# Optimization experiments

Hardware: AMD Instinct MI355X
Metric: run time of the kernel (lower is better)

## Reference

```python
import jax, jax.numpy as jnp
import numpy as np

SEQ_LEN = 8192
HEAD_DIM = 128


def setup_inputs() -> dict:
    key = jax.random.key(0)
    kq, kk, kv = jax.random.split(key, 3)
    q = jax.random.normal(kq, (SEQ_LEN, HEAD_DIM), dtype=jnp.float32)
    k = jax.random.normal(kk, (SEQ_LEN, HEAD_DIM), dtype=jnp.float32)
    v = jax.random.normal(kv, (SEQ_LEN, HEAD_DIM), dtype=jnp.float32)
    return {"q": q, "k": k, "v": v}


def reference(q, k, v):
    # FlashAttention computes exact softmax attention; the blocked loops with
    # online max/sum rescaling in the source are an exact reformulation of:
    #   O = softmax(Q K^T) V
    # NOTE: the original module applies no 1/sqrt(d) scaling, so neither do we.
    s = jnp.einsum('nd,md->nm', q, k)          # [N, N] scores
    p = jax.nn.softmax(s, axis=-1)             # stable softmax (online in src)
    return jnp.einsum('nm,md->nd', p, v)       # [N, d]
```

## Files before the change

### kernel.cpp

```cpp
#include <hip/hip_runtime.h>

#define N_SEQ 8192
#define HDIM  128

typedef _Float16 half8v  __attribute__((ext_vector_type(8)));
typedef float    floatx16 __attribute__((ext_vector_type(16)));
typedef unsigned int uint32;

__global__ void prep_kv(const float* __restrict__ K, const float* __restrict__ V,
                        _Float16* __restrict__ K16s, _Float16* __restrict__ Vs) {
    __shared__ float Kl[32 * 132];
    __shared__ float Vl[32 * 132];
    const int t  = threadIdx.x;
    const int nt = blockIdx.x;
    const int n0 = nt * 32;
    #pragma unroll
    for (int kk = 0; kk < 4; kk++) {
        int idx = t + 256 * kk;
        int nl = idx >> 5, c4 = idx & 31;
        float4 f = *(((const float4*)(K + (size_t)(n0 + nl) * HDIM)) + c4);
        float* dk = &Kl[nl * 132 + c4 * 4];
        dk[0] = f.x; dk[1] = f.y; dk[2] = f.z; dk[3] = f.w;
        float4 g = *(((const float4*)(V + (size_t)(n0 + nl) * HDIM)) + c4);
        float* dv = &Vl[nl * 132 + c4 * 4];
        dv[0] = g.x; dv[1] = g.y; dv[2] = g.z; dv[3] = g.w;
    }
    __syncthreads();
    #pragma unroll
    for (int rep = 0; rep < 2; rep++) {
        int ch = t + rep * 256;
        int kc = ch >> 6, lane = ch & 63, l31 = lane & 31, q5 = (lane >> 5) & 1;
        half8v h;
        #pragma unroll
        for (int j = 0; j < 8; j++) h[j] = (_Float16)Kl[l31 * 132 + kc * 16 + q5 * 8 + j];
        *(half8v*)(K16s + (((size_t)nt * 8 + kc) * 64 + lane) * 8) = h;
    }
    #pragma unroll
    for (int rep = 0; rep < 2; rep++) {
        int ch = t + rep * 256;
        int dt = ch >> 7, kc2 = (ch >> 6) & 1, lane = ch & 63, l31 = lane & 31, q5 = (lane >> 5) & 1;
        half8v h;
        #pragma unroll
        for (int j = 0; j < 8; j++) h[j] = (_Float16)Vl[(kc2 * 16 + q5 * 8 + j) * 132 + dt * 32 + l31];
        *(half8v*)(Vs + ((((size_t)nt * 4 + dt) * 2 + kc2) * 64 + lane) * 8) = h;
    }
}

__launch_bounds__(256, 2)
__global__ void fa_main(const float* __restrict__ Qp, const _Float16* __restrict__ K16s,
                        const _Float16* __restrict__ Vs, float* __restrict__ Opart,
                        float* __restrict__ lpart, float* __restrict__ mpart, int tiles) {
    const int tid  = threadIdx.x;
    const int lane = tid & 63;
    const int wv   = tid >> 6;
    const int l31  = lane & 31;
    const int q5   = lane >> 5;
    const int m0   = blockIdx.x * 128 + wv * 32;
    const int sp   = blockIdx.y;
    const float LOG2E = 1.44269504088896f;

    half8v qf[8];
    {
        const float* qrow = Qp + (size_t)(m0 + l31) * HDIM;
        #pragma unroll
        for (int kc = 0; kc < 8; kc++) {
            const float4 a = *(const float4*)(qrow + kc * 16 + q5 * 8);
            const float4 b = *(const float4*)(qrow + kc * 16 + q5 * 8 + 4);
            half8v h;
            h[0] = (_Float16)(a.x * LOG2E); h[1] = (_Float16)(a.y * LOG2E);
            h[2] = (_Float16)(a.z * LOG2E); h[3] = (_Float16)(a.w * LOG2E);
            h[4] = (_Float16)(b.x * LOG2E); h[5] = (_Float16)(b.y * LOG2E);
            h[6] = (_Float16)(b.z * LOG2E); h[7] = (_Float16)(b.w * LOG2E);
            qf[kc] = h;
        }
    }

    floatx16 oacc[4];
    #pragma unroll
    for (int dt = 0; dt < 4; dt++)
        #pragma unroll
        for (int r = 0; r < 16; r++) oacc[dt][r] = 0.0f;

    float runm = -3.0e38f;
    float lsum = 0.0f;

    const int nt0 = sp * tiles;
    for (int it = 0; it < tiles; ++it) {
        const size_t nt = nt0 + it;
        half8v vf[8];
        #pragma unroll
        for (int dt = 0; dt < 4; dt++)
            #pragma unroll
            for (int kc2 = 0; kc2 < 2; kc2++)
                vf[dt * 2 + kc2] = *(const half8v*)(Vs + (((nt * 4 + dt) * 2 + kc2) * 64 + lane) * 8);
        half8v kf[8];
        #pragma unroll
        for (int kc = 0; kc < 8; kc++)
            kf[kc] = *(const half8v*)(K16s + ((nt * 8 + kc) * 64 + lane) * 8);
        floatx16 s0, s1;
        #pragma unroll
        for (int r = 0; r < 16; r++) { s0[r] = 0.0f; s1[r] = 0.0f; }
        #pragma unroll
        for (int kc = 0; kc < 4; kc++)
            s0 = __builtin_amdgcn_mfma_f32_32x32x16_f16(kf[kc], qf[kc], s0, 0, 0, 0);
        #pragma unroll
        for (int kc = 4; kc < 8; kc++)
            s1 = __builtin_amdgcn_mfma_f32_32x32x16_f16(kf[kc], qf[kc], s1, 0, 0, 0);
        float sc[16];
        #pragma unroll
        for (int r = 0; r < 16; r++) sc[r] = s0[r] + s1[r];
        float tm[8];
        #pragma unroll
        for (int r = 0; r < 8; r++) tm[r] = fmaxf(sc[r], sc[r + 8]);
        #pragma unroll
        for (int w = 4; w; w >>= 1)
            #pragma unroll
            for (int r = 0; r < w; r++) tm[r] = fmaxf(tm[r], tm[r + w]);
        float cmax = fmaxf(tm[0], __shfl_xor(tm[0], 32, 64));
        if (__any(cmax > runm + 12.0f)) {
            const float mnew  = fmaxf(runm, cmax);
            const float alpha = __builtin_amdgcn_exp2f(runm - mnew);
            runm = mnew;
            lsum *= alpha;
            #pragma unroll
            for (int dt = 0; dt < 4; dt++)
                #pragma unroll
                for (int r = 0; r < 16; r++) oacc[dt][r] *= alpha;
        }
        float p[16];
        #pragma unroll
        for (int r = 0; r < 16; r++) p[r] = __builtin_amdgcn_exp2f(sc[r] - runm);
        float ts[8];
        #pragma unroll
        for (int r = 0; r < 8; r++) ts[r] = p[r] + p[r + 8];
        #pragma unroll
        for (int w = 4; w; w >>= 1)
            #pragma unroll
            for (int r = 0; r < w; r++) ts[r] += ts[r + w];
        lsum += ts[0];
        uint32 hpk[8];
        #pragma unroll
        for (int t2 = 0; t2 < 8; t2++) {
            auto pk = __builtin_amdgcn_cvt_pkrtz(p[2 * t2], p[2 * t2 + 1]);
            hpk[t2] = __builtin_bit_cast(uint32, pk);
        }
        #pragma unroll
        for (int kc2 = 0; kc2 < 2; kc2++) {
            uint32 pass0 = q5 ? hpk[4 * kc2 + 0] : hpk[4 * kc2 + 2];
            uint32 pass1 = q5 ? hpk[4 * kc2 + 1] : hpk[4 * kc2 + 3];
            uint32 r0 = (uint32)__shfl_xor((int)pass0, 32, 64);
            uint32 r1 = (uint32)__shfl_xor((int)pass1, 32, 64);
            uint32 b0 = q5 ? r0 : hpk[4 * kc2 + 0];
            uint32 b1 = q5 ? r1 : hpk[4 * kc2 + 1];
            uint32 b2 = q5 ? hpk[4 * kc2 + 2] : r0;
            uint32 b3 = q5 ? hpk[4 * kc2 + 3] : r1;
            uint4 bu = make_uint4(b0, b1, b2, b3);
            half8v bfrag = __builtin_bit_cast(half8v, bu);
            #pragma unroll
            for (int dt = 0; dt < 4; dt++)
                oacc[dt] = __builtin_amdgcn_mfma_f32_32x32x16_f16(vf[dt * 2 + kc2], bfrag, oacc[dt], 0, 0, 0);
        }
    }

    float ltot = lsum + __shfl_xor(lsum, 32, 64);
    if (lane < 32) {
        __builtin_nontemporal_store(ltot, &lpart[(size_t)sp * N_SEQ + m0 + l31]);
        __builtin_nontemporal_store(runm, &mpart[(size_t)sp * N_SEQ + m0 + l31]);
    }
    #pragma unroll
    for (int dt = 0; dt < 4; dt++)
        #pragma unroll
        for (int r = 0; r < 16; r++) {
            int d = dt * 32 + (r & 3) + 8 * (r >> 2) + 4 * q5;
            __builtin_nontemporal_store(oacc[dt][r],
                &Opart[((size_t)sp * HDIM + d) * N_SEQ + m0 + l31]);
        }
}

__global__ void fa_merge(const float* __restrict__ Opart, const float* __restrict__ lpart,
                         const float* __restrict__ mpart, float* __restrict__ Out, int S) {
    __shared__ float lds[64 * 33];
    const int t  = threadIdx.x;
    const int m0 = blockIdx.x * 64;
    const int i  = t & 63;
    const int g  = t >> 6;
    const int m  = m0 + i;
    const int d0 = blockIdx.y * 32 + g * 8;

    float M = -3.0e38f;
    for (int s = 0; s < S; s++) M = fmaxf(M, mpart[(size_t)s * N_SEQ + m]);
    float L = 0.0f;
    for (int s = 0; s < S; s++)
        L += lpart[(size_t)s * N_SEQ + m] * __builtin_amdgcn_exp2f(mpart[(size_t)s * N_SEQ + m] - M);
    const float inv = 1.0f / L;

    float acc[8];
    #pragma unroll
    for (int dd = 0; dd < 8; dd++) acc[dd] = 0.0f;
    for (int s = 0; s < S; s++) {
        const float ww = __builtin_amdgcn_exp2f(mpart[(size_t)s * N_SEQ + m] - M) * inv;
        #pragma unroll
        for (int dd = 0; dd < 8; dd++)
            acc[dd] += __builtin_nontemporal_load(
                &Opart[((size_t)s * HDIM + d0 + dd) * N_SEQ + m]) * ww;
    }
    #pragma unroll
    for (int dd = 0; dd < 8; dd++) lds[i * 33 + g * 8 + dd] = acc[dd];
    __syncthreads();
    const int mi = t >> 2, c = t & 3;
    float4 v0, v1;
    const float* row = &lds[mi * 33 + c * 8];
    v0.x = row[0]; v0.y = row[1]; v0.z = row[2]; v0.w = row[3];
    v1.x = row[4]; v1.y = row[5]; v1.z = row[6]; v1.w = row[7];
    float* outp = Out + (size_t)(m0 + mi) * HDIM + blockIdx.y * 32 + c * 8;
    *(float4*)(outp)     = v0;
    *(float4*)(outp + 4) = v1;
}

__global__ void fa_naive(const float* __restrict__ Q, const float* __restrict__ K,
                         const float* __restrict__ V, float* __restrict__ O) {
    const int m = blockIdx.x;
    const int t = threadIdx.x;
    __shared__ float qs[HDIM];
    __shared__ float ps[256];
    __shared__ float red[256];
    if (t < HDIM) qs[t] = Q[(size_t)m * HDIM + t] * 1.44269504f;
    __syncthreads();
    float om = -3.0e38f, ls = 0.0f, oa = 0.0f;
    for (int nb = 0; nb < N_SEQ; nb += 256) {
        const float* kr = K + (size_t)(nb + t) * HDIM;
        float s = 0.0f;
        #pragma unroll 8
        for (int d = 0; d < HDIM; d++) s += qs[d] * kr[d];
        red[t] = s; __syncthreads();
        for (int st = 128; st > 0; st >>= 1) { if (t < st) red[t] = fmaxf(red[t], red[t + st]); __syncthreads(); }
        float cm = red[0];
        __syncthreads();
        float mn = fmaxf(om, cm);
        float al = __builtin_amdgcn_exp2f(om - mn);
        om = mn;
        float pp = __builtin_amdgcn_exp2f(s - mn);
        ps[t] = pp; red[t] = pp; __syncthreads();
        for (int st = 128; st > 0; st >>= 1) { if (t < st) red[t] += red[t + st]; __syncthreads(); }
        float csum = red[0];
        ls = ls * al + csum;
        if (t < HDIM) {
            float acc = 0.0f;
            for (int j = 0; j < 256; j++) acc += ps[j] * V[(size_t)(nb + j) * HDIM + t];
            oa = oa * al + acc;
        }
        __syncthreads();
    }
    if (t < HDIM) O[(size_t)m * HDIM + t] = oa / ls;
}

extern "C" void kernel_launch(void* const* d_in, const int* in_sizes, int n_in,
                              void* d_out, int out_size, void* d_ws, size_t ws_size,
                              hipStream_t stream) {
    const float* q = (const float*)d_in[0];
    const float* k = (const float*)d_in[1];
    const float* v = (const float*)d_in[2];
    float* out = (float*)d_out;

    const size_t MB = 1024ull * 1024ull;
    int S = 0;
    for (int s = 8; s >= 1; s >>= 1) {
        size_t need = 4 * MB + (size_t)s * (4 * MB + 64 * 1024);
        if (ws_size >= need) { S = s; break; }
    }
    if (S == 0) {
        fa_naive<<<N_SEQ, 256, 0, stream>>>(q, k, v, out);
        return;
    }
    char* ws = (char*)d_ws;
    _Float16* K16s = (_Float16*)ws;
    _Float16* Vs   = (_Float16*)(ws + 2 * MB);
    float* Opart   = (float*)(ws + 4 * MB);
    float* lpart   = (float*)(ws + 4 * MB + (size_t)S * 4 * MB);
    float* mpart   = lpart + (size_t)S * N_SEQ;

    prep_kv<<<dim3(N_SEQ / 32), dim3(256), 0, stream>>>(k, v, K16s, Vs);
    fa_main<<<dim3(N_SEQ / 128, S), dim3(256), 0, stream>>>(q, K16s, Vs, Opart, lpart, mpart, (N_SEQ / 32) / S);
    fa_merge<<<dim3(N_SEQ / 64, HDIM / 32), dim3(256), 0, stream>>>(Opart, lpart, mpart, out, S);
}
```

Baseline: 128.8 us.

## Software-pipeline PV matmul one tile behind QK and softmax

Restructures the main attention loop so that the PV MFMA for tile i-1 is issued alongside the QK MFMA and softmax for tile i, using double-buffered V fragments and deferred rescaling of the output accumulator. The goal is to overlap exp/reduction VALU work and global loads with matrix-core work, rather than serialising them within each iteration. In exchange it raises register pressure under 2-wave occupancy bounds, and the loop now assumes an even tile count of at least 2.

```diff
diff --git a/kernel.cpp b/kernel.cpp
--- a/kernel.cpp
+++ b/kernel.cpp
@@ -43,6 +43,95 @@
         #pragma unroll
         for (int j = 0; j < 8; j++) h[j] = (_Float16)Vl[(kc2 * 16 + q5 * 8 + j) * 132 + dt * 32 + l31];
         *(half8v*)(Vs + ((((size_t)nt * 4 + dt) * 2 + kc2) * 64 + lane) * 8) = h;
+    }
+}
+
+static __device__ __forceinline__ void do_pv(const half8v (&vsrc)[8], const uint32 (&hpk)[8],
+                                             floatx16 (&oacc)[4], int q5) {
+    #pragma unroll
+    for (int kc2 = 0; kc2 < 2; kc2++) {
+        uint32 pass0 = q5 ? hpk[4 * kc2 + 0] : hpk[4 * kc2 + 2];
+        uint32 pass1 = q5 ? hpk[4 * kc2 + 1] : hpk[4 * kc2 + 3];
+        uint32 r0 = (uint32)__shfl_xor((int)pass0, 32, 64);
+        uint32 r1 = (uint32)__shfl_xor((int)pass1, 32, 64);
+        uint32 b0 = q5 ? r0 : hpk[4 * kc2 + 0];
+        uint32 b1 = q5 ? r1 : hpk[4 * kc2 + 1];
+        uint32 b2 = q5 ? hpk[4 * kc2 + 2] : r0;
+        uint32 b3 = q5 ? hpk[4 * kc2 + 3] : r1;
+        uint4 bu = make_uint4(b0, b1, b2, b3);
+        half8v bfrag = __builtin_bit_cast(half8v, bu);
+        #pragma unroll
+        for (int dt = 0; dt < 4; dt++)
+            oacc[dt] = __builtin_amdgcn_mfma_f32_32x32x16_f16(vsrc[dt * 2 + kc2], bfrag, oacc[dt], 0, 0, 0);
+    }
+}
+
+template <bool DO_PV>
+static __device__ __forceinline__ void pipe_step(
+        const half8v (&qf)[8], half8v (&vin)[8], const half8v (&vprev)[8],
+        floatx16 (&oacc)[4], uint32 (&hpk)[8],
+        float& runm, float& lsum, float& palpha, bool& pflag,
+        const _Float16* __restrict__ K16s, const _Float16* __restrict__ Vs,
+        size_t nt, int lane, int q5) {
+    half8v kf[8];
+    #pragma unroll
+    for (int kc = 0; kc < 8; kc++)
+        kf[kc] = *(const half8v*)(K16s + ((nt * 8 + kc) * 64 + lane) * 8);
+    #pragma unroll
+    for (int dt = 0; dt < 4; dt++)
+        #pragma unroll
+        for (int kc2 = 0; kc2 < 2; kc2++)
+            vin[dt * 2 + kc2] = *(const half8v*)(Vs + (((nt * 4 + dt) * 2 + kc2) * 64 + lane) * 8);
+    if (pflag) {
+        #pragma unroll
+        for (int dt = 0; dt < 4; dt++)
+            #pragma unroll
+            for (int r = 0; r < 16; r++) oacc[dt][r] *= palpha;
+        pflag = false;
+    }
+    if (DO_PV) do_pv(vprev, hpk, oacc, q5);
+    floatx16 s0, s1;
+    #pragma unroll
+    for (int r = 0; r < 16; r++) { s0[r] = 0.0f; s1[r] = 0.0f; }
+    #pragma unroll
+    for (int kc = 0; kc < 4; kc++)
+        s0 = __builtin_amdgcn_mfma_f32_32x32x16_f16(kf[kc], qf[kc], s0, 0, 0, 0);
+    #pragma unroll
+    for (int kc = 4; kc < 8; kc++)
+        s1 = __builtin_amdgcn_mfma_f32_32x32x16_f16(kf[kc], qf[kc], s1, 0, 0, 0);
+    float sc[16];
+    #pragma unroll
+    for (int r = 0; r < 16; r++) sc[r] = s0[r] + s1[r];
+    float tm[8];
+    #pragma unroll
+    for (int r = 0; r < 8; r++) tm[r] = fmaxf(sc[r], sc[r + 8]);
+    #pragma unroll
+    for (int w = 4; w; w >>= 1)
+        #pragma unroll
+        for (int r = 0; r < w; r++) tm[r] = fmaxf(tm[r], tm[r + w]);
+    float cmax = fmaxf(tm[0], __shfl_xor(tm[0], 32, 64));
+    if (__any(cmax > runm + 12.0f)) {
+        const float mnew = fmaxf(runm, cmax);
+        palpha = __builtin_amdgcn_exp2f(runm - mnew);
+        runm = mnew;
+        lsum *= palpha;
+        pflag = true;
+    }
+    float p[16];
+    #pragma unroll
+    for (int r = 0; r < 16; r++) p[r] = __builtin_amdgcn_exp2f(sc[r] - runm);
+    float ts[8];
+    #pragma unroll
+    for (int r = 0; r < 8; r++) ts[r] = p[r] + p[r + 8];
+    #pragma unroll
+    for (int w = 4; w; w >>= 1)
+        #pragma unroll
+        for (int r = 0; r < w; r++) ts[r] += ts[r + w];
+    lsum += ts[0];
+    #pragma unroll
+    for (int t2 = 0; t2 < 8; t2++) {
+        auto pk = __builtin_amdgcn_cvt_pkrtz(p[2 * t2], p[2 * t2 + 1]);
+        hpk[t2] = __builtin_bit_cast(uint32, pk);
     }
 }
 
@@ -83,84 +172,25 @@
 
     float runm = -3.0e38f;
     float lsum = 0.0f;
-
-    const int nt0 = sp * tiles;
-    for (int it = 0; it < tiles; ++it) {
-        const size_t nt = nt0 + it;
-        half8v vf[8];
+    float palpha = 0.0f;
+    bool  pflag = false;
+    uint32 hpk[8];
+    half8v va[8], vb[8];
+
+    const size_t nt0 = (size_t)sp * tiles;
+    pipe_step<false>(qf, va, va, oacc, hpk, runm, lsum, palpha, pflag, K16s, Vs, nt0, lane, q5);
+    for (int p = 0; p < (tiles - 2) / 2; p++) {
+        pipe_step<true>(qf, vb, va, oacc, hpk, runm, lsum, palpha, pflag, K16s, Vs, nt0 + 1 + 2 * p, lane, q5);
+        pipe_step<true>(qf, va, vb, oacc, hpk, runm, lsum, palpha, pflag, K16s, Vs, nt0 + 2 + 2 * p, lane, q5);
+    }
+    pipe_step<true>(qf, vb, va, oacc, hpk, runm, lsum, palpha, pflag, K16s, Vs, nt0 + tiles - 1, lane, q5);
+    if (pflag) {
         #pragma unroll
         for (int dt = 0; dt < 4; dt++)
             #pragma unroll
-            for (int kc2 = 0; kc2 < 2; kc2++)
-                vf[dt * 2 + kc2] = *(const half8v*)(Vs + (((nt * 4 + dt) * 2 + kc2) * 64 + lane) * 8);
-        half8v kf[8];
-        #pragma unroll
-        for (int kc = 0; kc < 8; kc++)
-            kf[kc] = *(const half8v*)(K16s + ((nt * 8 + kc) * 64 + lane) * 8);
-        floatx16 s0, s1;
-        #pragma unroll
-        for (int r = 0; r < 16; r++) { s0[r] = 0.0f; s1[r] = 0.0f; }
-        #pragma unroll
-        for (int kc = 0; kc < 4; kc++)
-            s0 = __builtin_amdgcn_mfma_f32_32x32x16_f16(kf[kc], qf[kc], s0, 0, 0, 0);
-        #pragma unroll
-        for (int kc = 4; kc < 8; kc++)
-            s1 = __builtin_amdgcn_mfma_f32_32x32x16_f16(kf[kc], qf[kc], s1, 0, 0, 0);
-        float sc[16];
-        #pragma unroll
-        for (int r = 0; r < 16; r++) sc[r] = s0[r] + s1[r];
-        float tm[8];
-        #pragma unroll
-        for (int r = 0; r < 8; r++) tm[r] = fmaxf(sc[r], sc[r + 8]);
-        #pragma unroll
-        for (int w = 4; w; w >>= 1)
-            #pragma unroll
-            for (int r = 0; r < w; r++) tm[r] = fmaxf(tm[r], tm[r + w]);
-        float cmax = fmaxf(tm[0], __shfl_xor(tm[0], 32, 64));
-        if (__any(cmax > runm + 12.0f)) {
-            const float mnew  = fmaxf(runm, cmax);
-            const float alpha = __builtin_amdgcn_exp2f(runm - mnew);
-            runm = mnew;
-            lsum *= alpha;
-            #pragma unroll
-            for (int dt = 0; dt < 4; dt++)
-                #pragma unroll
-                for (int r = 0; r < 16; r++) oacc[dt][r] *= alpha;
-        }
-        float p[16];
-        #pragma unroll
-        for (int r = 0; r < 16; r++) p[r] = __builtin_amdgcn_exp2f(sc[r] - runm);
-        float ts[8];
-        #pragma unroll
-        for (int r = 0; r < 8; r++) ts[r] = p[r] + p[r + 8];
-        #pragma unroll
-        for (int w = 4; w; w >>= 1)
-            #pragma unroll
-            for (int r = 0; r < w; r++) ts[r] += ts[r + w];
-        lsum += ts[0];
-        uint32 hpk[8];
-        #pragma unroll
-        for (int t2 = 0; t2 < 8; t2++) {
-            auto pk = __builtin_amdgcn_cvt_pkrtz(p[2 * t2], p[2 * t2 + 1]);
-            hpk[t2] = __builtin_bit_cast(uint32, pk);
-        }
-        #pragma unroll
-        for (int kc2 = 0; kc2 < 2; kc2++) {
-            uint32 pass0 = q5 ? hpk[4 * kc2 + 0] : hpk[4 * kc2 + 2];
-            uint32 pass1 = q5 ? hpk[4 * kc2 + 1] : hpk[4 * kc2 + 3];
-            uint32 r0 = (uint32)__shfl_xor((int)pass0, 32, 64);
-            uint32 r1 = (uint32)__shfl_xor((int)pass1, 32, 64);
-            uint32 b0 = q5 ? r0 : hpk[4 * kc2 + 0];
-            uint32 b1 = q5 ? r1 : hpk[4 * kc2 + 1];
-            uint32 b2 = q5 ? hpk[4 * kc2 + 2] : r0;
-            uint32 b3 = q5 ? hpk[4 * kc2 + 3] : r1;
-            uint4 bu = make_uint4(b0, b1, b2, b3);
-            half8v bfrag = __builtin_bit_cast(half8v, bu);
-            #pragma unroll
-            for (int dt = 0; dt < 4; dt++)
-                oacc[dt] = __builtin_amdgcn_mfma_f32_32x32x16_f16(vf[dt * 2 + kc2], bfrag, oacc[dt], 0, 0, 0);
-        }
-    }
+            for (int r = 0; r < 16; r++) oacc[dt][r] *= palpha;
+    }
+    do_pv(vb, hpk, oacc, q5);
 
     float ltot = lsum + __shfl_xor(lsum, 32, 64);
     if (lane < 32) {
```

Result: no change. 126.7 us (-1.6%).
